# Optimization experiments

Measured on AMD Instinct MI355X. Metric: run time of the kernel, lower is better.

## Reference

```python
import jax, jax.numpy as jnp
import numpy as np

N_V = 100000
N_E = 20000
NNZ = 1600000
D = 128


def setup_inputs() -> dict:
    key = jax.random.key(0)
    k1, k2, k3, k4, k5 = jax.random.split(key, 5)
    X = jax.random.normal(k1, (N_V, D), dtype=jnp.float32)
    W = jax.random.normal(k2, (D, D), dtype=jnp.float32) * (1.0 / np.sqrt(D))
    b = jax.random.normal(k3, (D,), dtype=jnp.float32) * 0.01
    v2e_src = jax.random.randint(k4, (NNZ,), 0, N_V, dtype=jnp.int32)
    v2e_dst = jax.random.randint(k5, (NNZ,), 0, N_E, dtype=jnp.int32)
    return {"X": X, "W": W, "b": b, "v2e_src": v2e_src, "v2e_dst": v2e_dst, "num_e": N_E}


def reference(X, W, b, v2e_src, v2e_dst, num_e):
    num_v = X.shape[0]
    ones = jnp.ones(v2e_src.shape[0], dtype=X.dtype)
    # node degrees (values of D_v diagonal) and hyperedge incidence counts
    deg_v = jax.ops.segment_sum(ones, v2e_src, num_segments=num_v)
    cnt_e = jax.ops.segment_sum(ones, v2e_dst, num_segments=num_e)

    # theta: linear layer
    Xt = X @ W.T + b  # [N_V, D]

    # v2e mean aggregation: per hyperedge, mean of incident vertex features
    Ysum = jax.ops.segment_sum(Xt[v2e_src], v2e_dst, num_segments=num_e)  # [N_E, D]
    Y = Ysum / jnp.maximum(cnt_e, 1.0)[:, None]

    # edge norm: torch scatter_reduce(reduce='mean', include_self=True) -> sum/(count+1)
    De_sum = jax.ops.segment_sum(deg_v[v2e_src], v2e_dst, num_segments=num_e)
    De = De_sum / (cnt_e + 1.0)
    De = jnp.where(De > 0, jax.lax.rsqrt(jnp.maximum(De, 1e-30)), 1.0)  # inf -> 1
    Y = De[:, None] * Y

    # e2v sum aggregation
    Xo = jax.ops.segment_sum(Y[v2e_dst], v2e_src, num_segments=num_v)  # [N_V, D]

    # D_v^{-1/2} sparse diagonal mm (zero-degree nodes -> 0)
    dvn = jnp.where(deg_v > 0, jax.lax.rsqrt(jnp.maximum(deg_v, 1e-30)), 0.0)
    Xo = dvn[:, None] * Xo

    # is_last=False: ReLU then dropout (dropout is identity in eval)
    return jax.nn.relu(Xo)
```

## Files before the change

### kernel.cpp

```cpp
#include <hip/hip_runtime.h>
#include <hip/hip_bf16.h>

#define NV 100000
#define NE 20000
#define DD 128
#define ESHIFT 7
#define VSHIFT 9
#define NBE 157
#define NBV 196
#define NBK 256
#define CHUNK 4096
#define CAPE 11264
#define CAPV 9216

using bf16 = __hip_bfloat16;

typedef __attribute__((ext_vector_type(8))) short frag_ab;
typedef __attribute__((ext_vector_type(4))) float frag_cd;

__device__ __forceinline__ float uas(unsigned u) { union { unsigned u; float f; } c; c.u = u; return c.f; }
__device__ __forceinline__ unsigned pk2(float lo, float hi) {
    bf16 l = __float2bfloat16(lo), h = __float2bfloat16(hi);
    return (unsigned)(*(unsigned short*)&l) | ((unsigned)(*(unsigned short*)&h) << 16);
}
__device__ __forceinline__ void accum8(float* a, uint4 x) {
    a[0] += uas(x.x << 16); a[1] += uas(x.x & 0xffff0000u);
    a[2] += uas(x.y << 16); a[3] += uas(x.y & 0xffff0000u);
    a[4] += uas(x.z << 16); a[5] += uas(x.z & 0xffff0000u);
    a[6] += uas(x.w << 16); a[7] += uas(x.w & 0xffff0000u);
}

__global__ void init_cur(int* __restrict__ bcur_e, int* __restrict__ bcur_v) {
    int t = threadIdx.x;
    bcur_e[t] = t * CAPE;
    bcur_v[t] = t * CAPV;
}

__global__ __launch_bounds__(256) void partition_and_cvt(const int* __restrict__ src, const int* __restrict__ dst,
                                                         int* __restrict__ bcur_e, int* __restrict__ bcur_v,
                                                         unsigned* __restrict__ pairs_e, unsigned* __restrict__ pairs_v,
                                                         int nnz,
                                                         const float4* __restrict__ Xf, ushort4* __restrict__ Xb,
                                                         const float4* __restrict__ Wf, ushort4* __restrict__ Wb) {
    int nchunk = (nnz + CHUNK - 1) / CHUNK;
    int t = threadIdx.x;
    if ((int)blockIdx.x >= nchunk) {
        const int n4x = NV * DD / 4;
        const int n4w = DD * DD / 4;
        int i = ((int)blockIdx.x - nchunk) * 256 + t;
        if (i < n4x + n4w) {
            float4 v;
            ushort4 o;
            if (i < n4x) v = Xf[i]; else v = Wf[i - n4x];
            bf16 a = __float2bfloat16(v.x); o.x = *(unsigned short*)&a;
            bf16 b = __float2bfloat16(v.y); o.y = *(unsigned short*)&b;
            bf16 c = __float2bfloat16(v.z); o.z = *(unsigned short*)&c;
            bf16 d = __float2bfloat16(v.w); o.w = *(unsigned short*)&d;
            if (i < n4x) Xb[i] = o; else Wb[i - n4x] = o;
        }
        return;
    }
    __shared__ int cntA[NBK], cntB[NBK], pre1[NBK], tot[NBK], sc[NBK], loff[NBK], gbase[NBK];
    __shared__ unsigned stage[CHUNK];
    int sub = t >> 7;
    int base = blockIdx.x * CHUNK;
    unsigned p[16];
    int rk[16];
#pragma unroll
    for (int k = 0; k < 16; ++k) {
        int i = base + k * 256 + t;
        p[k] = (i < nnz) ? (((unsigned)src[i] << 15) | (unsigned)dst[i]) : 0xFFFFFFFFu;
    }

    cntA[t] = 0; cntB[t] = 0;
    __syncthreads();
#pragma unroll
    for (int k = 0; k < 16; ++k)
        if (p[k] != 0xFFFFFFFFu) {
            int b = (p[k] >> ESHIFT) & 0xFF;
            rk[k] = atomicAdd(sub ? &cntB[b] : &cntA[b], 1);
        }
    __syncthreads();
    {
        int a = cntA[t], b = cntB[t];
        pre1[t] = a; tot[t] = a + b; sc[t] = a + b;
    }
    __syncthreads();
    for (int o = 1; o < NBK; o <<= 1) { int x = (t >= o) ? sc[t - o] : 0; __syncthreads(); sc[t] += x; __syncthreads(); }
    loff[t] = sc[t] - tot[t];
    gbase[t] = (tot[t] > 0) ? atomicAdd(&bcur_e[t], tot[t]) : 0;
    __syncthreads();
#pragma unroll
    for (int k = 0; k < 16; ++k)
        if (p[k] != 0xFFFFFFFFu) {
            int b = (p[k] >> ESHIFT) & 0xFF;
            stage[loff[b] + rk[k] + (sub ? pre1[b] : 0)] = p[k];
        }
    __syncthreads();
    {
        int wid = t >> 6, ln = t & 63;
        for (int b2 = wid; b2 < NBK; b2 += 4) {
            int n = tot[b2], lo = loff[b2], gb = gbase[b2];
            for (int idx = ln; idx < n; idx += 64) pairs_e[gb + idx] = stage[lo + idx];
        }
    }
    __syncthreads();

    cntA[t] = 0; cntB[t] = 0;
    __syncthreads();
#pragma unroll
    for (int k = 0; k < 16; ++k)
        if (p[k] != 0xFFFFFFFFu) {
            int b = p[k] >> 24;
            rk[k] = atomicAdd(sub ? &cntB[b] : &cntA[b], 1);
        }
    __syncthreads();
    {
        int a = cntA[t], b = cntB[t];
        pre1[t] = a; tot[t] = a + b; sc[t] = a + b;
    }
    __syncthreads();
    for (int o = 1; o < NBK; o <<= 1) { int x = (t >= o) ? sc[t - o] : 0; __syncthreads(); sc[t] += x; __syncthreads(); }
    loff[t] = sc[t] - tot[t];
    gbase[t] = (tot[t] > 0) ? atomicAdd(&bcur_v[t], tot[t]) : 0;
    __syncthreads();
#pragma unroll
    for (int k = 0; k < 16; ++k)
        if (p[k] != 0xFFFFFFFFu) {
            int b = p[k] >> 24;
            stage[loff[b] + rk[k] + (sub ? pre1[b] : 0)] = p[k];
        }
    __syncthreads();
    {
        int wid = t >> 6, ln = t & 63;
        for (int b2 = wid; b2 < NBK; b2 += 4) {
            int n = tot[b2], lo = loff[b2], gb = gbase[b2];
            for (int idx = ln; idx < n; idx += 64) pairs_v[gb + idx] = stage[lo + idx];
        }
    }
}

__global__ __launch_bounds__(1024) void build_csr(const unsigned* __restrict__ pairs_e, const int* __restrict__ bcur_e,
                                                  int* __restrict__ off_e, int* __restrict__ end_e, int* __restrict__ e_src,
                                                  const unsigned* __restrict__ pairs_v, const int* __restrict__ bcur_v,
                                                  int* __restrict__ off_v, int* __restrict__ end_v, int* __restrict__ v_edge,
                                                  int* __restrict__ deg_v) {
    __shared__ int cA[2048], cB[2048], sc2[512], eoff[512];
    int t = threadIdx.x;
    cA[t] = 0; cA[t + 1024] = 0;
    __syncthreads();
    if ((int)blockIdx.x < NBE) {
        int b = blockIdx.x;
        int lo = b * CAPE, hi = bcur_e[b];
        int sub = t >> 7;
        unsigned pv[12];
        int rk[12];
        int kk = 0;
        for (int i = lo + t; i < hi; i += 1024, ++kk) {
            unsigned p = pairs_e[i];
            pv[kk] = p;
            rk[kk] = atomicAdd(&cA[sub * 128 + (p & 127)], 1);
        }
        __syncthreads();
        if (t < 128) {
            int run = 0;
#pragma unroll
            for (int s = 0; s < 8; ++s) { cB[s * 128 + t] = run; run += cA[s * 128 + t]; }
            sc2[t] = run;
        }
        __syncthreads();
        for (int o = 1; o < 128; o <<= 1) {
            int x = 0;
            if (t < 128 && t >= o) x = sc2[t - o];
            __syncthreads();
            if (t < 128) sc2[t] += x;
            __syncthreads();
        }
        if (t < 128) {
            int totalb = cB[7 * 128 + t] + cA[7 * 128 + t];
            int ex = sc2[t] - totalb;
            eoff[t] = ex;
            int e = (b << ESHIFT) + t;
            if (e < NE) { off_e[e] = lo + ex; end_e[e] = lo + ex + totalb; }
        }
        __syncthreads();
        for (int k = 0; k < kk; ++k) {
            int bkt = pv[k] & 127;
            int pos = lo + eoff[bkt] + cB[sub * 128 + bkt] + rk[k];
            e_src[pos] = (int)(pv[k] >> 15);
        }
    } else {
        int b = blockIdx.x - NBE;
        int lo = b * CAPV, hi = bcur_v[b];
        int sub = t >> 8;
        unsigned pv[9];
        int rk[9];
        int kk = 0;
        for (int i = lo + t; i < hi; i += 1024, ++kk) {
            unsigned p = pairs_v[i];
            pv[kk] = p;
            rk[kk] = atomicAdd(&cA[sub * 512 + ((p >> 15) & 511)], 1);
        }
        __syncthreads();
        if (t < 512) {
            int run = 0;
#pragma unroll
            for (int s = 0; s < 4; ++s) { cB[s * 512 + t] = run; run += cA[s * 512 + t]; }
            sc2[t] = run;
        }
        __syncthreads();
        for (int o = 1; o < 512; o <<= 1) {
            int x = 0;
            if (t < 512 && t >= o) x = sc2[t - o];
            __syncthreads();
            if (t < 512) sc2[t] += x;
            __syncthreads();
        }
        if (t < 512) {
            int totalb = cB[3 * 512 + t] + cA[3 * 512 + t];
            int ex = sc2[t] - totalb;
            eoff[t] = ex;
            int v = (b << VSHIFT) + t;
            if (v < NV) { off_v[v] = lo + ex; end_v[v] = lo + ex + totalb; deg_v[v] = totalb; }
        }
        __syncthreads();
        for (int k = 0; k < kk; ++k) {
            int bkt = (pv[k] >> 15) & 511;
            int pos = lo + eoff[bkt] + cB[sub * 512 + bkt] + rk[k];
            v_edge[pos] = (int)(pv[k] & 0x7FFF);
        }
    }
}

__global__ __launch_bounds__(256) void edge_fused(const uint4* __restrict__ Xq, const int* __restrict__ off_e,
                                                  const int* __restrict__ end_e,
                                                  const int* __restrict__ e_src, const int* __restrict__ deg_v,
                                                  const bf16* __restrict__ Wb, const float* __restrict__ bias,
                                                  bf16* __restrict__ Y) {
    __shared__ short Stile[16][136];
    __shared__ float betaL[16];
    int t = threadIdx.x;
    int w = t >> 6, lane = t & 63;
    int g = lane >> 4, l16 = lane & 15;
    int mBase = blockIdx.x * 16;

    for (int ei = 0; ei < 4; ++ei) {
        int le = w * 4 + ei;
        int e = mBase + le;
        int start = off_e[e], end = end_e[e];
        float acc[8] = {0.f, 0.f, 0.f, 0.f, 0.f, 0.f, 0.f, 0.f};
        float degsum = 0.f;
        int j = start;
        for (; j + 16 <= end; j += 16) {
            int s0 = e_src[j + g];
            int s1 = e_src[j + 4 + g];
            int s2 = e_src[j + 8 + g];
            int s3 = e_src[j + 12 + g];
            uint4 x0 = Xq[(size_t)s0 * 16 + l16];
            uint4 x1 = Xq[(size_t)s1 * 16 + l16];
            uint4 x2 = Xq[(size_t)s2 * 16 + l16];
            uint4 x3 = Xq[(size_t)s3 * 16 + l16];
            degsum += (float)(deg_v[s0] + deg_v[s1] + deg_v[s2] + deg_v[s3]);
            accum8(acc, x0);
            accum8(acc, x1);
            accum8(acc, x2);
            accum8(acc, x3);
        }
        for (; j < end; j += 4) {
            int idx = j + g;
            if (idx < end) {
                int s = e_src[idx];
                uint4 x = Xq[(size_t)s * 16 + l16];
                degsum += (float)deg_v[s];
                accum8(acc, x);
            }
        }
#pragma unroll
        for (int i = 0; i < 8; ++i) {
            acc[i] += __shfl_xor(acc[i], 16);
            acc[i] += __shfl_xor(acc[i], 32);
        }
        degsum += __shfl_xor(degsum, 16);
        degsum += __shfl_xor(degsum, 32);

        float cntf = (float)(end - start);
        float Des = degsum / (cntf + 1.0f);
        float De = (Des > 0.f) ? rsqrtf(fmaxf(Des, 1e-30f)) : 1.0f;
        float scale = De / fmaxf(cntf, 1.0f);
        if (g == 0) {
            uint4 o;
            o.x = pk2(acc[0] * scale, acc[1] * scale);
            o.y = pk2(acc[2] * scale, acc[3] * scale);
            o.z = pk2(acc[4] * scale, acc[5] * scale);
            o.w = pk2(acc[6] * scale, acc[7] * scale);
            *(uint4*)&Stile[le][l16 * 8] = o;
            if (l16 == 0) betaL[le] = (cntf > 0.f) ? De : 0.f;
        }
    }
    __syncthreads();

    const short* Ws = (const short*)Wb;
    int quad = g;
    frag_ab a[4];
#pragma unroll
    for (int kt = 0; kt < 4; ++kt)
        a[kt] = *(const frag_ab*)&Stile[l16][kt * 32 + quad * 8];
    float beta_r[4];
#pragma unroll
    for (int r = 0; r < 4; ++r) beta_r[r] = betaL[quad * 4 + r];

#pragma unroll
    for (int nn = 0; nn < 2; ++nn) {
        int nt = w * 2 + nn;
        frag_cd acc = {0.f, 0.f, 0.f, 0.f};
#pragma unroll
        for (int kt = 0; kt < 4; ++kt) {
            frag_ab bfr = *(const frag_ab*)(Ws + (size_t)(nt * 16 + l16) * DD + kt * 32 + quad * 8);
            acc = __builtin_amdgcn_mfma_f32_16x16x32_bf16(a[kt], bfr, acc, 0, 0, 0);
        }
        float bv = bias[nt * 16 + l16];
#pragma unroll
        for (int r = 0; r < 4; ++r) {
            int row = mBase + quad * 4 + r;
            float v = acc[r] + beta_r[r] * bv;
            Y[(size_t)row * DD + nt * 16 + l16] = __float2bfloat16(v);
        }
    }
}

__global__ __launch_bounds__(256) void vertex_agg(const uint4* __restrict__ Yq, const int* __restrict__ off_v,
                                                  const int* __restrict__ end_v,
                                                  const int* __restrict__ v_edge, float* __restrict__ out) {
    int wave = (blockIdx.x * blockDim.x + threadIdx.x) >> 6;
    int lane = threadIdx.x & 63;
    if (wave >= NV) return;
    int g = lane >> 4, l16 = lane & 15;
    int start = off_v[wave], end = end_v[wave];
    float acc[8] = {0.f, 0.f, 0.f, 0.f, 0.f, 0.f, 0.f, 0.f};
    int j = start;
    for (; j + 16 <= end; j += 16) {
        int e0 = v_edge[j + g];
        int e1 = v_edge[j + 4 + g];
        int e2 = v_edge[j + 8 + g];
        int e3 = v_edge[j + 12 + g];
        uint4 y0 = Yq[(size_t)e0 * 16 + l16];
        uint4 y1 = Yq[(size_t)e1 * 16 + l16];
        uint4 y2 = Yq[(size_t)e2 * 16 + l16];
        uint4 y3 = Yq[(size_t)e3 * 16 + l16];
        accum8(acc, y0);
        accum8(acc, y1);
        accum8(acc, y2);
        accum8(acc, y3);
    }
    for (; j < end; j += 4) {
        int idx = j + g;
        if (idx < end) {
            int e = v_edge[idx];
            uint4 y = Yq[(size_t)e * 16 + l16];
            accum8(acc, y);
        }
    }
#pragma unroll
    for (int i = 0; i < 8; ++i) {
        acc[i] += __shfl_xor(acc[i], 16);
        acc[i] += __shfl_xor(acc[i], 32);
    }
    int deg = end - start;
    float dvn = (deg > 0) ? rsqrtf((float)deg) : 0.f;
    if (g == 0) {
        float4 o1, o2;
        o1.x = fmaxf(acc[0] * dvn, 0.f);
        o1.y = fmaxf(acc[1] * dvn, 0.f);
        o1.z = fmaxf(acc[2] * dvn, 0.f);
        o1.w = fmaxf(acc[3] * dvn, 0.f);
        o2.x = fmaxf(acc[4] * dvn, 0.f);
        o2.y = fmaxf(acc[5] * dvn, 0.f);
        o2.z = fmaxf(acc[6] * dvn, 0.f);
        o2.w = fmaxf(acc[7] * dvn, 0.f);
        float4* op = (float4*)(out + (size_t)wave * DD + l16 * 8);
        op[0] = o1;
        op[1] = o2;
    }
}

extern "C" void kernel_launch(void* const* d_in, const int* in_sizes, int n_in,
                              void* d_out, int out_size, void* d_ws, size_t ws_size,
                              hipStream_t stream) {
    const float* X = (const float*)d_in[0];
    const float* W = (const float*)d_in[1];
    const float* b = (const float*)d_in[2];
    const int* src = (const int*)d_in[3];
    const int* dst = (const int*)d_in[4];
    int nnz = in_sizes[3];

    char* ws = (char*)d_ws;
    size_t o = 0;
    auto take = [&](size_t bytes) -> char* {
        char* p = ws + o;
        o += (bytes + 255) & ~(size_t)255;
        return p;
    };
    int* bcur_e = (int*)take(NBK * 4);
    int* bcur_v = (int*)take(NBK * 4);
    int* off_e = (int*)take((size_t)NE * 4);
    int* end_e = (int*)take((size_t)NE * 4);
    int* off_v = (int*)take((size_t)NV * 4);
    int* end_v = (int*)take((size_t)NV * 4);
    int* deg_v = (int*)take((size_t)NV * 4);
    int* e_src = (int*)take((size_t)NBE * CAPE * 4);
    int* v_edge = (int*)take((size_t)NBV * CAPV * 4);
    unsigned* pairs_e = (unsigned*)take((size_t)NBE * CAPE * 4);
    unsigned* pairs_v = (unsigned*)take((size_t)NBV * CAPV * 4);
    bf16* Y = (bf16*)take((size_t)NE * DD * 2);
    bf16* Wb = (bf16*)take((size_t)DD * DD * 2);
    bf16* Xb = (bf16*)take((size_t)NV * DD * 2);
    (void)ws_size; (void)n_in; (void)out_size;

    int nchunk = (nnz + CHUNK - 1) / CHUNK;
    int ncvt = (NV * DD / 4 + DD * DD / 4 + 255) / 256;

    init_cur<<<1, NBK, 0, stream>>>(bcur_e, bcur_v);
    partition_and_cvt<<<nchunk + ncvt, 256, 0, stream>>>(src, dst, bcur_e, bcur_v, pairs_e, pairs_v, nnz,
                                                         (const float4*)X, (ushort4*)Xb,
                                                         (const float4*)W, (ushort4*)Wb);
    build_csr<<<NBE + NBV, 1024, 0, stream>>>(pairs_e, bcur_e, off_e, end_e, e_src,
                                              pairs_v, bcur_v, off_v, end_v, v_edge, deg_v);
    edge_fused<<<NE / 16, 256, 0, stream>>>((const uint4*)Xb, off_e, end_e, e_src, deg_v, Wb, b, Y);
    vertex_agg<<<NV * 64 / 256, 256, 0, stream>>>((const uint4*)Y, off_v, end_v, v_edge, (float*)d_out);
}
```

Measured before the change: 268.0 us.

## Use wave-shuffle scans and assign one row per 16-lane group in gathers

Replaces the shared-memory Hillis-Steele scans in the partition and CSR-build kernels with wave-level shuffle scans plus a small cross-wave fixup, and flattens the staged copy-out loop to one pass over all valid entries. In the edge and vertex aggregation kernels, each 16-lane group now owns a whole edge or vertex instead of a wave splitting one row four ways. This removes the cross-group shuffle reduction and lets the vertex kernel launch a quarter as many waves. The cost is more divergence across groups when row lengths differ, and each group walks its index list serially.

```diff
diff --git a/kernel.cpp b/kernel.cpp
--- a/kernel.cpp
+++ b/kernel.cpp
@@ -28,6 +28,14 @@
     a[2] += uas(x.y << 16); a[3] += uas(x.y & 0xffff0000u);
     a[4] += uas(x.z << 16); a[5] += uas(x.z & 0xffff0000u);
     a[6] += uas(x.w << 16); a[7] += uas(x.w & 0xffff0000u);
+}
+__device__ __forceinline__ int wave_incl_scan(int v, int lane) {
+#pragma unroll
+    for (int o = 1; o < 64; o <<= 1) {
+        int x = __shfl_up(v, o);
+        if (lane >= o) v += x;
+    }
+    return v;
 }
 
 __global__ void init_cur(int* __restrict__ bcur_e, int* __restrict__ bcur_v) {
@@ -60,9 +68,11 @@
         }
         return;
     }
-    __shared__ int cntA[NBK], cntB[NBK], pre1[NBK], tot[NBK], sc[NBK], loff[NBK], gbase[NBK];
+    __shared__ int cntA[NBK], cntB[NBK], pre1[NBK], loff[NBK], gbase[NBK], wsum[4];
+    __shared__ int totValid;
     __shared__ unsigned stage[CHUNK];
     int sub = t >> 7;
+    int lane = t & 63, wv = t >> 6;
     int base = blockIdx.x * CHUNK;
     unsigned p[16];
     int rk[16];
@@ -82,13 +92,19 @@
         }
     __syncthreads();
     {
-        int a = cntA[t], b = cntB[t];
-        pre1[t] = a; tot[t] = a + b; sc[t] = a + b;
-    }
-    __syncthreads();
-    for (int o = 1; o < NBK; o <<= 1) { int x = (t >= o) ? sc[t - o] : 0; __syncthreads(); sc[t] += x; __syncthreads(); }
-    loff[t] = sc[t] - tot[t];
-    gbase[t] = (tot[t] > 0) ? atomicAdd(&bcur_e[t], tot[t]) : 0;
+        int a = cntA[t], bb = cntB[t];
+        int tv = a + bb;
+        pre1[t] = a;
+        int incl = wave_incl_scan(tv, lane);
+        if (lane == 63) wsum[wv] = incl;
+        __syncthreads();
+        if (t == 0) { int r = 0; for (int i = 0; i < 4; ++i) { int x = wsum[i]; wsum[i] = r; r += x; } }
+        __syncthreads();
+        int ex = incl - tv + wsum[wv];
+        loff[t] = ex;
+        gbase[t] = (tv > 0) ? atomicAdd(&bcur_e[t], tv) : 0;
+        if (t == 255) totValid = ex + tv;
+    }
     __syncthreads();
 #pragma unroll
     for (int k = 0; k < 16; ++k)
@@ -97,12 +113,10 @@
             stage[loff[b] + rk[k] + (sub ? pre1[b] : 0)] = p[k];
         }
     __syncthreads();
-    {
-        int wid = t >> 6, ln = t & 63;
-        for (int b2 = wid; b2 < NBK; b2 += 4) {
-            int n = tot[b2], lo = loff[b2], gb = gbase[b2];
-            for (int idx = ln; idx < n; idx += 64) pairs_e[gb + idx] = stage[lo + idx];
-        }
+    for (int i = t; i < totValid; i += 256) {
+        unsigned pp = stage[i];
+        int b = (pp >> ESHIFT) & 0xFF;
+        pairs_e[gbase[b] + i - loff[b]] = pp;
     }
     __syncthreads();
 
@@ -116,13 +130,19 @@
         }
     __syncthreads();
     {
-        int a = cntA[t], b = cntB[t];
-        pre1[t] = a; tot[t] = a + b; sc[t] = a + b;
-    }
-    __syncthreads();
-    for (int o = 1; o < NBK; o <<= 1) { int x = (t >= o) ? sc[t - o] : 0; __syncthreads(); sc[t] += x; __syncthreads(); }
-    loff[t] = sc[t] - tot[t];
-    gbase[t] = (tot[t] > 0) ? atomicAdd(&bcur_v[t], tot[t]) : 0;
+        int a = cntA[t], bb = cntB[t];
+        int tv = a + bb;
+        pre1[t] = a;
+        int incl = wave_incl_scan(tv, lane);
+        if (lane == 63) wsum[wv] = incl;
+        __syncthreads();
+        if (t == 0) { int r = 0; for (int i = 0; i < 4; ++i) { int x = wsum[i]; wsum[i] = r; r += x; } }
+        __syncthreads();
+        int ex = incl - tv + wsum[wv];
+        loff[t] = ex;
+        gbase[t] = (tv > 0) ? atomicAdd(&bcur_v[t], tv) : 0;
+        if (t == 255) totValid = ex + tv;
+    }
     __syncthreads();
 #pragma unroll
     for (int k = 0; k < 16; ++k)
@@ -131,12 +151,10 @@
             stage[loff[b] + rk[k] + (sub ? pre1[b] : 0)] = p[k];
         }
     __syncthreads();
-    {
-        int wid = t >> 6, ln = t & 63;
-        for (int b2 = wid; b2 < NBK; b2 += 4) {
-            int n = tot[b2], lo = loff[b2], gb = gbase[b2];
-            for (int idx = ln; idx < n; idx += 64) pairs_v[gb + idx] = stage[lo + idx];
-        }
+    for (int i = t; i < totValid; i += 256) {
+        unsigned pp = stage[i];
+        int b = pp >> 24;
+        pairs_v[gbase[b] + i - loff[b]] = pp;
     }
 }
 
@@ -145,7 +163,7 @@
                                                   const unsigned* __restrict__ pairs_v, const int* __restrict__ bcur_v,
                                                   int* __restrict__ off_v, int* __restrict__ end_v, int* __restrict__ v_edge,
                                                   int* __restrict__ deg_v) {
-    __shared__ int cA[2048], cB[2048], sc2[512], eoff[512];
+    __shared__ int cA[2048], cB[2048], sc2[512], eoff[512], wsumS[8];
     int t = threadIdx.x;
     cA[t] = 0; cA[t + 1024] = 0;
     __syncthreads();
@@ -169,19 +187,20 @@
             sc2[t] = run;
         }
         __syncthreads();
-        for (int o = 1; o < 128; o <<= 1) {
-            int x = 0;
-            if (t < 128 && t >= o) x = sc2[t - o];
-            __syncthreads();
-            if (t < 128) sc2[t] += x;
-            __syncthreads();
-        }
+        int incl = 0, myrun = 0;
         if (t < 128) {
-            int totalb = cB[7 * 128 + t] + cA[7 * 128 + t];
-            int ex = sc2[t] - totalb;
+            myrun = sc2[t];
+            incl = wave_incl_scan(myrun, t & 63);
+            if ((t & 63) == 63) wsumS[t >> 6] = incl;
+        }
+        __syncthreads();
+        if (t == 0) { int r = 0; for (int i = 0; i < 2; ++i) { int x = wsumS[i]; wsumS[i] = r; r += x; } }
+        __syncthreads();
+        if (t < 128) {
+            int ex = incl - myrun + wsumS[t >> 6];
             eoff[t] = ex;
             int e = (b << ESHIFT) + t;
-            if (e < NE) { off_e[e] = lo + ex; end_e[e] = lo + ex + totalb; }
+            if (e < NE) { off_e[e] = lo + ex; end_e[e] = lo + ex + myrun; }
         }
         __syncthreads();
         for (int k = 0; k < kk; ++k) {
@@ -209,19 +228,20 @@
             sc2[t] = run;
         }
         __syncthreads();
-        for (int o = 1; o < 512; o <<= 1) {
-            int x = 0;
-            if (t < 512 && t >= o) x = sc2[t - o];
-            __syncthreads();
-            if (t < 512) sc2[t] += x;
-            __syncthreads();
-        }
+        int incl = 0, myrun = 0;
         if (t < 512) {
-            int totalb = cB[3 * 512 + t] + cA[3 * 512 + t];
-            int ex = sc2[t] - totalb;
+            myrun = sc2[t];
+            incl = wave_incl_scan(myrun, t & 63);
+            if ((t & 63) == 63) wsumS[t >> 6] = incl;
+        }
+        __syncthreads();
+        if (t == 0) { int r = 0; for (int i = 0; i < 8; ++i) { int x = wsumS[i]; wsumS[i] = r; r += x; } }
+        __syncthreads();
+        if (t < 512) {
+            int ex = incl - myrun + wsumS[t >> 6];
             eoff[t] = ex;
             int v = (b << VSHIFT) + t;
-            if (v < NV) { off_v[v] = lo + ex; end_v[v] = lo + ex + totalb; deg_v[v] = totalb; }
+            if (v < NV) { off_v[v] = lo + ex; end_v[v] = lo + ex + myrun; deg_v[v] = myrun; }
         }
         __syncthreads();
         for (int k = 0; k < kk; ++k) {
@@ -243,59 +263,55 @@
     int w = t >> 6, lane = t & 63;
     int g = lane >> 4, l16 = lane & 15;
     int mBase = blockIdx.x * 16;
-
-    for (int ei = 0; ei < 4; ++ei) {
-        int le = w * 4 + ei;
-        int e = mBase + le;
-        int start = off_e[e], end = end_e[e];
-        float acc[8] = {0.f, 0.f, 0.f, 0.f, 0.f, 0.f, 0.f, 0.f};
-        float degsum = 0.f;
-        int j = start;
-        for (; j + 16 <= end; j += 16) {
-            int s0 = e_src[j + g];
-            int s1 = e_src[j + 4 + g];
-            int s2 = e_src[j + 8 + g];
-            int s3 = e_src[j + 12 + g];
-            uint4 x0 = Xq[(size_t)s0 * 16 + l16];
-            uint4 x1 = Xq[(size_t)s1 * 16 + l16];
-            uint4 x2 = Xq[(size_t)s2 * 16 + l16];
-            uint4 x3 = Xq[(size_t)s3 * 16 + l16];
-            degsum += (float)(deg_v[s0] + deg_v[s1] + deg_v[s2] + deg_v[s3]);
-            accum8(acc, x0);
-            accum8(acc, x1);
-            accum8(acc, x2);
-            accum8(acc, x3);
-        }
-        for (; j < end; j += 4) {
-            int idx = j + g;
-            if (idx < end) {
-                int s = e_src[idx];
-                uint4 x = Xq[(size_t)s * 16 + l16];
-                degsum += (float)deg_v[s];
-                accum8(acc, x);
-            }
-        }
-#pragma unroll
-        for (int i = 0; i < 8; ++i) {
-            acc[i] += __shfl_xor(acc[i], 16);
-            acc[i] += __shfl_xor(acc[i], 32);
-        }
-        degsum += __shfl_xor(degsum, 16);
-        degsum += __shfl_xor(degsum, 32);
-
-        float cntf = (float)(end - start);
-        float Des = degsum / (cntf + 1.0f);
-        float De = (Des > 0.f) ? rsqrtf(fmaxf(Des, 1e-30f)) : 1.0f;
-        float scale = De / fmaxf(cntf, 1.0f);
-        if (g == 0) {
-            uint4 o;
-            o.x = pk2(acc[0] * scale, acc[1] * scale);
-            o.y = pk2(acc[2] * scale, acc[3] * scale);
-            o.z = pk2(acc[4] * scale, acc[5] * scale);
-            o.w = pk2(acc[6] * scale, acc[7] * scale);
-            *(uint4*)&Stile[le][l16 * 8] = o;
-            if (l16 == 0) betaL[le] = (cntf > 0.f) ? De : 0.f;
-        }
+    int le = w * 4 + g;
+    int e = mBase + le;
+    int start = off_e[e], end = end_e[e];
+    float acc[8] = {0.f, 0.f, 0.f, 0.f, 0.f, 0.f, 0.f, 0.f};
+    float degsum = 0.f;
+    int j = start;
+    for (; j + 8 <= end; j += 8) {
+        int s0 = e_src[j + 0], s1 = e_src[j + 1], s2 = e_src[j + 2], s3 = e_src[j + 3];
+        int s4 = e_src[j + 4], s5 = e_src[j + 5], s6 = e_src[j + 6], s7 = e_src[j + 7];
+        uint4 x0 = Xq[(size_t)s0 * 16 + l16];
+        uint4 x1 = Xq[(size_t)s1 * 16 + l16];
+        uint4 x2 = Xq[(size_t)s2 * 16 + l16];
+        uint4 x3 = Xq[(size_t)s3 * 16 + l16];
+        uint4 x4 = Xq[(size_t)s4 * 16 + l16];
+        uint4 x5 = Xq[(size_t)s5 * 16 + l16];
+        uint4 x6 = Xq[(size_t)s6 * 16 + l16];
+        uint4 x7 = Xq[(size_t)s7 * 16 + l16];
+        degsum += (float)(deg_v[s0] + deg_v[s1] + deg_v[s2] + deg_v[s3]
+                        + deg_v[s4] + deg_v[s5] + deg_v[s6] + deg_v[s7]);
+        accum8(acc, x0); accum8(acc, x1); accum8(acc, x2); accum8(acc, x3);
+        accum8(acc, x4); accum8(acc, x5); accum8(acc, x6); accum8(acc, x7);
+    }
+    for (; j + 4 <= end; j += 4) {
+        int s0 = e_src[j + 0], s1 = e_src[j + 1], s2 = e_src[j + 2], s3 = e_src[j + 3];
+        uint4 x0 = Xq[(size_t)s0 * 16 + l16];
+        uint4 x1 = Xq[(size_t)s1 * 16 + l16];
+        uint4 x2 = Xq[(size_t)s2 * 16 + l16];
+        uint4 x3 = Xq[(size_t)s3 * 16 + l16];
+        degsum += (float)(deg_v[s0] + deg_v[s1] + deg_v[s2] + deg_v[s3]);
+        accum8(acc, x0); accum8(acc, x1); accum8(acc, x2); accum8(acc, x3);
+    }
+    for (; j < end; ++j) {
+        int s = e_src[j];
+        uint4 x = Xq[(size_t)s * 16 + l16];
+        degsum += (float)deg_v[s];
+        accum8(acc, x);
+    }
+    float cntf = (float)(end - start);
+    float Des = degsum / (cntf + 1.0f);
+    float De = (Des > 0.f) ? rsqrtf(fmaxf(Des, 1e-30f)) : 1.0f;
+    float scale = De / fmaxf(cntf, 1.0f);
+    {
+        uint4 o;
+        o.x = pk2(acc[0] * scale, acc[1] * scale);
+        o.y = pk2(acc[2] * scale, acc[3] * scale);
+        o.z = pk2(acc[4] * scale, acc[5] * scale);
+        o.w = pk2(acc[6] * scale, acc[7] * scale);
+        *(uint4*)&Stile[le][l16 * 8] = o;
+        if (l16 == 0) betaL[le] = (cntf > 0.f) ? De : 0.f;
     }
     __syncthreads();
 
@@ -312,17 +328,17 @@
 #pragma unroll
     for (int nn = 0; nn < 2; ++nn) {
         int nt = w * 2 + nn;
-        frag_cd acc = {0.f, 0.f, 0.f, 0.f};
+        frag_cd acc2 = {0.f, 0.f, 0.f, 0.f};
 #pragma unroll
         for (int kt = 0; kt < 4; ++kt) {
             frag_ab bfr = *(const frag_ab*)(Ws + (size_t)(nt * 16 + l16) * DD + kt * 32 + quad * 8);
-            acc = __builtin_amdgcn_mfma_f32_16x16x32_bf16(a[kt], bfr, acc, 0, 0, 0);
+            acc2 = __builtin_amdgcn_mfma_f32_16x16x32_bf16(a[kt], bfr, acc2, 0, 0, 0);
         }
         float bv = bias[nt * 16 + l16];
 #pragma unroll
         for (int r = 0; r < 4; ++r) {
             int row = mBase + quad * 4 + r;
-            float v = acc[r] + beta_r[r] * bv;
+            float v = acc2[r] + beta_r[r] * bv;
             Y[(size_t)row * DD + nt * 16 + l16] = __float2bfloat16(v);
         }
     }
@@ -333,54 +349,53 @@
                                                   const int* __restrict__ v_edge, float* __restrict__ out) {
     int wave = (blockIdx.x * blockDim.x + threadIdx.x) >> 6;
     int lane = threadIdx.x & 63;
-    if (wave >= NV) return;
     int g = lane >> 4, l16 = lane & 15;
-    int start = off_v[wave], end = end_v[wave];
+    int v = wave * 4 + g;
+    if (v >= NV) return;
+    int start = off_v[v], end = end_v[v];
     float acc[8] = {0.f, 0.f, 0.f, 0.f, 0.f, 0.f, 0.f, 0.f};
     int j = start;
-    for (; j + 16 <= end; j += 16) {
-        int e0 = v_edge[j + g];
-        int e1 = v_edge[j + 4 + g];
-        int e2 = v_edge[j + 8 + g];
-        int e3 = v_edge[j + 12 + g];
+    for (; j + 8 <= end; j += 8) {
+        int e0 = v_edge[j + 0], e1 = v_edge[j + 1], e2 = v_edge[j + 2], e3 = v_edge[j + 3];
+        int e4 = v_edge[j + 4], e5 = v_edge[j + 5], e6 = v_edge[j + 6], e7 = v_edge[j + 7];
         uint4 y0 = Yq[(size_t)e0 * 16 + l16];
         uint4 y1 = Yq[(size_t)e1 * 16 + l16];
         uint4 y2 = Yq[(size_t)e2 * 16 + l16];
         uint4 y3 = Yq[(size_t)e3 * 16 + l16];
-        accum8(acc, y0);
-        accum8(acc, y1);
-        accum8(acc, y2);
-        accum8(acc, y3);
-    }
-    for (; j < end; j += 4) {
-        int idx = j + g;
-        if (idx < end) {
-            int e = v_edge[idx];
-            uint4 y = Yq[(size_t)e * 16 + l16];
-            accum8(acc, y);
-        }
-    }
-#pragma unroll
-    for (int i = 0; i < 8; ++i) {
-        acc[i] += __shfl_xor(acc[i], 16);
-        acc[i] += __shfl_xor(acc[i], 32);
+        uint4 y4 = Yq[(size_t)e4 * 16 + l16];
+        uint4 y5 = Yq[(size_t)e5 * 16 + l16];
+        uint4 y6 = Yq[(size_t)e6 * 16 + l16];
+        uint4 y7 = Yq[(size_t)e7 * 16 + l16];
+        accum8(acc, y0); accum8(acc, y1); accum8(acc, y2); accum8(acc, y3);
+        accum8(acc, y4); accum8(acc, y5); accum8(acc, y6); accum8(acc, y7);
+    }
+    for (; j + 4 <= end; j += 4) {
+        int e0 = v_edge[j + 0], e1 = v_edge[j + 1], e2 = v_edge[j + 2], e3 = v_edge[j + 3];
+        uint4 y0 = Yq[(size_t)e0 * 16 + l16];
+        uint4 y1 = Yq[(size_t)e1 * 16 + l16];
+        uint4 y2 = Yq[(size_t)e2 * 16 + l16];
+        uint4 y3 = Yq[(size_t)e3 * 16 + l16];
+        accum8(acc, y0); accum8(acc, y1); accum8(acc, y2); accum8(acc, y3);
+    }
+    for (; j < end; ++j) {
+        int e = v_edge[j];
+        uint4 y = Yq[(size_t)e * 16 + l16];
+        accum8(acc, y);
     }
     int deg = end - start;
     float dvn = (deg > 0) ? rsqrtf((float)deg) : 0.f;
-    if (g == 0) {
-        float4 o1, o2;
-        o1.x = fmaxf(acc[0] * dvn, 0.f);
-        o1.y = fmaxf(acc[1] * dvn, 0.f);
-        o1.z = fmaxf(acc[2] * dvn, 0.f);
-        o1.w = fmaxf(acc[3] * dvn, 0.f);
-        o2.x = fmaxf(acc[4] * dvn, 0.f);
-        o2.y = fmaxf(acc[5] * dvn, 0.f);
-        o2.z = fmaxf(acc[6] * dvn, 0.f);
-        o2.w = fmaxf(acc[7] * dvn, 0.f);
-        float4* op = (float4*)(out + (size_t)wave * DD + l16 * 8);
-        op[0] = o1;
-        op[1] = o2;
-    }
+    float4 o1, o2;
+    o1.x = fmaxf(acc[0] * dvn, 0.f);
+    o1.y = fmaxf(acc[1] * dvn, 0.f);
+    o1.z = fmaxf(acc[2] * dvn, 0.f);
+    o1.w = fmaxf(acc[3] * dvn, 0.f);
+    o2.x = fmaxf(acc[4] * dvn, 0.f);
+    o2.y = fmaxf(acc[5] * dvn, 0.f);
+    o2.z = fmaxf(acc[6] * dvn, 0.f);
+    o2.w = fmaxf(acc[7] * dvn, 0.f);
+    float4* op = (float4*)(out + (size_t)v * DD + l16 * 8);
+    op[0] = o1;
+    op[1] = o2;
 }
 
 extern "C" void kernel_launch(void* const* d_in, const int* in_sizes, int n_in,
@@ -426,5 +441,5 @@
     build_csr<<<NBE + NBV, 1024, 0, stream>>>(pairs_e, bcur_e, off_e, end_e, e_src,
                                               pairs_v, bcur_v, off_v, end_v, v_edge, deg_v);
     edge_fused<<<NE / 16, 256, 0, stream>>>((const uint4*)Xb, off_e, end_e, e_src, deg_v, Wb, b, Y);
-    vertex_agg<<<NV * 64 / 256, 256, 0, stream>>>((const uint4*)Y, off_v, end_v, v_edge, (float*)d_out);
-}
+    vertex_agg<<<(NV / 4 * 64) / 256, 256, 0, stream>>>((const uint4*)Y, off_v, end_v, v_edge, (float*)d_out);
+}
```

After: 256.1 us. 1.05x faster.
